# Optimization experiments

Measured on AMD Instinct MI355X. Metric: run time of the kernel, lower is better.

Reference implementation:

```python
import jax, jax.numpy as jnp
import numpy as np

R = 4  # search_radius


def conv3(x, w, b):
    # 3x3 conv, padding=1 (SAME), NCHW / OIHW
    y = jax.lax.conv_general_dilated(x, w, window_strides=(1, 1), padding='SAME',
                                     dimension_numbers=('NCHW', 'OIHW', 'NCHW'))
    return y + b[None, :, None, None]


def bilinear_border(img, x, y):
    # torch F.grid_sample(mode='bilinear', padding_mode='border', align_corners=True)
    # img: (B,C,H,W); x,y: (B,H,W) unnormalized pixel coords
    B, C, H, W = img.shape
    x = jnp.clip(x, 0.0, W - 1.0)
    y = jnp.clip(y, 0.0, H - 1.0)
    x0 = jnp.floor(x)
    y0 = jnp.floor(y)
    x0i = x0.astype(jnp.int32)
    y0i = y0.astype(jnp.int32)
    x1i = jnp.minimum(x0i + 1, W - 1)
    y1i = jnp.minimum(y0i + 1, H - 1)
    wx = (x - x0)[..., None]
    wy = (y - y0)[..., None]
    imgt = jnp.transpose(img, (0, 2, 3, 1))  # (B,H,W,C)
    b = jnp.arange(B)[:, None, None]
    v00 = imgt[b, y0i, x0i]
    v01 = imgt[b, y0i, x1i]
    v10 = imgt[b, y1i, x0i]
    v11 = imgt[b, y1i, x1i]
    out = (v00 * (1 - wx) + v01 * wx) * (1 - wy) + (v10 * (1 - wx) + v11 * wx) * wy
    return jnp.transpose(out, (0, 3, 1, 2))


def _forward(feat1, feat2, initial_flow,
             fW1, fb1, fW2, fb2, fW3, fb3,
             rW1, rb1, rW2, rb2, rW3, rb3, rW4, rb4):
    relu = jax.nn.relu

    def extract(x):
        x = relu(conv3(x, fW1, fb1))
        x = relu(conv3(x, fW2, fb2))
        return relu(conv3(x, fW3, fb3))  # (B, 32, H, W)

    f1 = extract(feat1)
    f2 = extract(feat2)
    B, C, H, W = f1.shape
    yy, xx = jnp.meshgrid(jnp.arange(H, dtype=jnp.float32),
                          jnp.arange(W, dtype=jnp.float32), indexing='ij')
    # warp feat2 by initial flow; align_corners=True normalization cancels -> pixel coords + flow
    f2w = bilinear_border(f2, xx[None] + initial_flow[:, 0], yy[None] + initial_flow[:, 1])
    # search offsets, same order as search_grid.view(2,-1).t(): (dx, dy) row-major over (dy rows)
    coords = jnp.arange(-R, R + 1, dtype=jnp.float32)
    gy, gx = jnp.meshgrid(coords, coords, indexing='ij')
    offs = jnp.stack([gx.reshape(-1), gy.reshape(-1)], axis=1)  # (81, 2)
    xb = jnp.broadcast_to(xx[None], (B, H, W))
    yb = jnp.broadcast_to(yy[None], (B, H, W))

    def cost_fn(off):
        shifted = bilinear_border(f2w, xb + off[0], yb + off[1])
        return jnp.sum(f1 * shifted, axis=1)  # (B,H,W)

    cv = jnp.transpose(jax.lax.map(cost_fn, offs), (1, 0, 2, 3))  # (B,81,H,W)
    h = jnp.concatenate([cv, initial_flow], axis=1)  # (B,83,H,W)
    h = relu(conv3(h, rW1, rb1))
    h = relu(conv3(h, rW2, rb2))
    h = relu(conv3(h, rW3, rb3))
    return initial_flow + conv3(h, rW4, rb4)


def setup_inputs():
    key = jax.random.key(0)
    ks = jax.random.split(key, 12)
    B, H, W = 2, 256, 448
    FC = 64
    CV = (2 * R + 1) ** 2  # 81
    s = 0.05
    d = {}
    d['feat1'] = jax.random.normal(ks[0], (B, 3, H, W), jnp.float32)
    d['feat2'] = jax.random.normal(ks[1], (B, 3, H, W), jnp.float32)
    d['initial_flow'] = jax.random.normal(ks[2], (B, 2, H, W), jnp.float32)
    d['fW1'] = jax.random.normal(ks[3], (FC, 3, 3, 3), jnp.float32) * s
    d['fb1'] = jnp.zeros((FC,), jnp.float32)
    d['fW2'] = jax.random.normal(ks[4], (FC, FC, 3, 3), jnp.float32) * s
    d['fb2'] = jnp.zeros((FC,), jnp.float32)
    d['fW3'] = jax.random.normal(ks[5], (FC // 2, FC, 3, 3), jnp.float32) * s
    d['fb3'] = jnp.zeros((FC // 2,), jnp.float32)
    d['rW1'] = jax.random.normal(ks[6], (128, CV + 2, 3, 3), jnp.float32) * s
    d['rb1'] = jnp.zeros((128,), jnp.float32)
    d['rW2'] = jax.random.normal(ks[7], (128, 128, 3, 3), jnp.float32) * s
    d['rb2'] = jnp.zeros((128,), jnp.float32)
    d['rW3'] = jax.random.normal(ks[8], (64, 128, 3, 3), jnp.float32) * s
    d['rb3'] = jnp.zeros((64,), jnp.float32)
    d['rW4'] = jax.random.normal(ks[9], (2, 64, 3, 3), jnp.float32) * s
    d['rb4'] = jnp.zeros((2,), jnp.float32)
    return d


def reference(feat1, feat2, initial_flow,
              fW1, fb1, fW2, fb2, fW3, fb3,
              rW1, rb1, rW2, rb2, rW3, rb3, rW4, rb4):
    return _forward(feat1, feat2, initial_flow,
                    fW1, fb1, fW2, fb2, fW3, fb3,
                    rW1, rb1, rW2, rb2, rW3, rb3, rW4, rb4)
```

## Files before the change

### kernel.cpp

```cpp
#include <hip/hip_runtime.h>

#define HH 256
#define WW 448
#define HW (HH * WW)

typedef short bf16x8 __attribute__((ext_vector_type(8)));
typedef float f32x4 __attribute__((ext_vector_type(4)));
typedef unsigned int uint32;
typedef unsigned short ushort;

__device__ __forceinline__ ushort f2bf(float f) {
    uint32 u = __float_as_uint(f);
    u += 0x7fffu + ((u >> 16) & 1u);
    return (ushort)(u >> 16);
}

__device__ __forceinline__ void pack_one(
    int i, const float* __restrict__ w, ushort* __restrict__ wp,
    int CinReal, int CinPad, int Cout)
{
    int total = 9 * CinPad * Cout;
    if (i >= total) return;
    int ci = i & 31;
    int rest = i >> 5;
    int n = rest % Cout;
    int rest2 = rest / Cout;
    int KC = CinPad / 32;
    int kc = rest2 % KC;
    int tap = rest2 / KC;
    int cin = kc * 32 + ci;
    float v = (cin < CinReal) ? w[((size_t)n * CinReal + cin) * 9 + tap] : 0.f;
    wp[i] = f2bf(v);
}

__global__ __launch_bounds__(256) void pack_all_k(
    const float* fW2, const float* fW3, const float* rW1,
    const float* rW2, const float* rW3,
    ushort* wp2, ushort* wp3, ushort* wpr1, ushort* wpr2, ushort* wpr3)
{
    int i = blockIdx.x * 256 + threadIdx.x;
    pack_one(i, fW2, wp2, 64, 64, 64);
    pack_one(i, fW3, wp3, 64, 64, 32);
    pack_one(i, rW1, wpr1, 83, 96, 128);
    pack_one(i, rW2, wpr2, 128, 128, 128);
    pack_one(i, rW3, wpr3, 128, 128, 64);
}

template <int CIN, int COUT, int RELU>
__global__ __launch_bounds__(256, 4) void convmfma_k(
    const ushort* __restrict__ in, const ushort* __restrict__ wp,
    const float* __restrict__ bias, ushort* __restrict__ out,
    long inStride, long outStride)
{
    constexpr int KC = CIN / 32;
    constexpr int NPH = (CIN + 63) / 64;
    constexpr int CS = 72;
    constexpr int NG = (COUT >= 128) ? 4 : 2;
    constexpr int WN = (COUT / 16) / NG;
    constexpr int MG = 4 / NG;
    constexpr int WM = 8 / MG;

    __shared__ __align__(16) ushort lds[180 * CS];

    const int tid = threadIdx.x;
    const int x0 = blockIdx.x * 16;
    const int y0 = blockIdx.y * 8;
    in += (size_t)blockIdx.z * inStride;
    out += (size_t)blockIdx.z * outStride;

    const int wv = tid >> 6;
    const int lane = tid & 63;
    const int m = lane & 15;
    const int quad = lane >> 4;
    const int mbase = (wv % MG) * WM;
    const int nbase = (wv / MG) * WN * 16;

    const ushort* ldsA = lds + (mbase * 18 + m) * CS + quad * 8;
    const ushort* wpB = wp + ((size_t)nbase + m) * 32 + quad * 8;

    f32x4 acc[WM][WN];
#pragma unroll
    for (int t = 0; t < WM; ++t)
#pragma unroll
        for (int u = 0; u < WN; ++u)
            acc[t][u] = (f32x4){0.f, 0.f, 0.f, 0.f};

#pragma unroll 1
    for (int ph = 0; ph < NPH; ++ph) {
        const int C = (CIN - ph * 64 >= 64) ? 64 : (CIN - ph * 64);
        const int sh = (C == 64) ? 3 : 2;
        const int ch8 = C >> 3;

        if (ph) __syncthreads();
        for (int i = tid; i < 180 * ch8; i += 256) {
            int p = i >> sh, c8 = i & (ch8 - 1);
            int ry = p / 18, rx = p - ry * 18;
            int gy = y0 + ry - 1, gx = x0 + rx - 1;
            float4 v = make_float4(0.f, 0.f, 0.f, 0.f);
            if (gy >= 0 && gy < HH && gx >= 0 && gx < WW)
                v = *(const float4*)(in + ((size_t)gy * WW + gx) * CIN + ph * 64 + c8 * 8);
            *(float4*)(lds + p * CS + c8 * 8) = v;
        }
        __syncthreads();

        const int KCc = C / 32;
        const ushort* wpP = wpB + (size_t)(ph * 2) * COUT * 32;
#pragma unroll 1
        for (int tap = 0; tap < 9; ++tap) {
            const int ky = tap / 3;
            const int kx = tap - 3 * ky;
            const ushort* wpT = wpP + (size_t)tap * KC * COUT * 32;
#pragma unroll
            for (int kc = 0; kc < 2; ++kc) {
                if (kc >= KCc) break;
                bf16x8 b[WN];
#pragma unroll
                for (int u = 0; u < WN; ++u)
                    b[u] = *(const bf16x8*)(wpT + ((size_t)kc * COUT + u * 16) * 32);
#pragma unroll
                for (int th = 0; th < WM / 4; ++th) {
                    bf16x8 a[4];
#pragma unroll
                    for (int t4 = 0; t4 < 4; ++t4)
                        a[t4] = *(const bf16x8*)(ldsA +
                                ((th * 4 + t4 + ky) * 18 + kx) * CS + kc * 32);
#pragma unroll
                    for (int t4 = 0; t4 < 4; ++t4)
#pragma unroll
                        for (int u = 0; u < WN; ++u)
                            acc[th * 4 + t4][u] =
                                __builtin_amdgcn_mfma_f32_16x16x32_bf16(
                                    a[t4], b[u], acc[th * 4 + t4][u], 0, 0, 0);
                }
            }
        }
    }

#pragma unroll
    for (int u = 0; u < WN; ++u) {
        const int n = nbase + u * 16 + m;
        const float bs = bias[n];
#pragma unroll
        for (int t = 0; t < WM; ++t) {
            const int y = y0 + mbase + t;
#pragma unroll
            for (int r = 0; r < 4; ++r) {
                const int x = x0 + quad * 4 + r;
                float v = acc[t][u][r] + bs;
                if (RELU) v = fmaxf(v, 0.f);
                out[((size_t)y * WW + x) * COUT + n] = f2bf(v);
            }
        }
    }
}

__global__ __launch_bounds__(256) void fconv1_k(
    const float* __restrict__ f1src, const float* __restrict__ f2src,
    const float* __restrict__ w, const float* __restrict__ bias,
    ushort* __restrict__ out, long inStride, long outStride)
{
    __shared__ float wl[1728];
    __shared__ float patch[3][4][18];
    const int tid = threadIdx.x;
    const int x0 = blockIdx.x * 16, y0 = blockIdx.y * 2;
    const int z = blockIdx.z;
    const float* in = ((z & 1) ? f2src : f1src) + (size_t)(z >> 1) * inStride;
    out += (size_t)z * outStride;
    for (int i = tid; i < 1728; i += 256) wl[i] = w[i];
    for (int i = tid; i < 216; i += 256) {
        int ci = i / 72;
        int r = (i - ci * 72) / 18;
        int c = i - ci * 72 - r * 18;
        int gy = y0 + r - 1, gx = x0 + c - 1;
        patch[ci][r][c] = (gy >= 0 && gy < HH && gx >= 0 && gx < WW)
                              ? in[(size_t)ci * HW + gy * WW + gx] : 0.f;
    }
    __syncthreads();
    const int g = tid & 7;
    const int p = tid >> 3;
    const int py = p >> 4, px = p & 15;
    float acc[8];
#pragma unroll
    for (int j = 0; j < 8; ++j) acc[j] = bias[g * 8 + j];
#pragma unroll
    for (int ci = 0; ci < 3; ++ci)
#pragma unroll
        for (int k = 0; k < 9; ++k) {
            const int ky = k / 3, kx = k - 3 * ky;
            const float v = patch[ci][py + ky][px + kx];
#pragma unroll
            for (int j = 0; j < 8; ++j)
                acc[j] = fmaf(v, wl[(g * 8 + j) * 27 + ci * 9 + k], acc[j]);
        }
    ushort ov[8];
#pragma unroll
    for (int j = 0; j < 8; ++j) ov[j] = f2bf(fmaxf(acc[j], 0.f));
    const int y = y0 + py, x = x0 + px;
    *(float4*)(out + ((size_t)y * WW + x) * 64 + g * 8) = *(const float4*)ov;
}

__global__ __launch_bounds__(256) void warp_k(
    const ushort* __restrict__ f2, const float* __restrict__ flow,
    ushort* __restrict__ outp, long fStride, long flowStride, long oStride)
{
    int idx = blockIdx.x * 256 + threadIdx.x;
    if (idx >= HW) return;
    f2 += (size_t)blockIdx.y * fStride;
    flow += (size_t)blockIdx.y * flowStride;
    outp += (size_t)blockIdx.y * oStride;
    int y = idx / WW, x = idx - y * WW;
    float px_ = (float)x + flow[idx];
    float py_ = (float)y + flow[idx + HW];
    px_ = fminf(fmaxf(px_, 0.f), (float)(WW - 1));
    py_ = fminf(fmaxf(py_, 0.f), (float)(HH - 1));
    float fx0 = floorf(px_), fy0 = floorf(py_);
    int xi0 = (int)fx0, yi0 = (int)fy0;
    int xi1 = min(xi0 + 1, WW - 1), yi1 = min(yi0 + 1, HH - 1);
    float wx = px_ - fx0, wy = py_ - fy0;
    float w00 = (1.f - wx) * (1.f - wy), w01 = wx * (1.f - wy);
    float w10 = (1.f - wx) * wy, w11 = wx * wy;

    const uint32* a = (const uint32*)(f2 + ((size_t)yi0 * WW + xi0) * 32);
    const uint32* b = (const uint32*)(f2 + ((size_t)yi0 * WW + xi1) * 32);
    const uint32* c = (const uint32*)(f2 + ((size_t)yi1 * WW + xi0) * 32);
    const uint32* d = (const uint32*)(f2 + ((size_t)yi1 * WW + xi1) * 32);
    uint32 ov[16];
#pragma unroll
    for (int i = 0; i < 16; ++i) {
        uint32 wa = a[i], wb = b[i], wc = c[i], wd = d[i];
        float lo = __uint_as_float(wa << 16) * w00 + __uint_as_float(wb << 16) * w01 +
                   __uint_as_float(wc << 16) * w10 + __uint_as_float(wd << 16) * w11;
        float hi = __uint_as_float(wa & 0xffff0000u) * w00 + __uint_as_float(wb & 0xffff0000u) * w01 +
                   __uint_as_float(wc & 0xffff0000u) * w10 + __uint_as_float(wd & 0xffff0000u) * w11;
        ov[i] = ((uint32)f2bf(hi) << 16) | f2bf(lo);
    }
    uint32* o = (uint32*)(outp + (size_t)idx * 32);
#pragma unroll
    for (int i = 0; i < 16; ++i) o[i] = ov[i];
}

__global__ __launch_bounds__(256) void cost_mfma_k(
    const ushort* __restrict__ f1, const ushort* __restrict__ f2w,
    const float* __restrict__ flow, ushort* __restrict__ hb,
    long f1S, long f2wS, long hbS, long flowS)
{
    const int tid = threadIdx.x;
    const int wv = tid >> 6;
    const int lane = tid & 63;
    const int c = lane & 15;
    const int quad = lane >> 4;
    const int x0 = blockIdx.x * 16;
    const int y = blockIdx.y * 4 + wv;
    f1 += (size_t)blockIdx.z * f1S;
    f2w += (size_t)blockIdx.z * f2wS;
    hb += (size_t)blockIdx.z * hbS;
    flow += (size_t)blockIdx.z * flowS;

    const bf16x8 a = *(const bf16x8*)(f1 + ((size_t)y * WW + x0 + c) * 32 + quad * 8);

    const int xc0 = min(max(x0 - 4 + c, 0), WW - 1);
    const int xc1 = min(max(x0 + 12 + c, 0), WW - 1);

    ushort* hrow = hb + ((size_t)y * WW + x0) * 96;

#pragma unroll 1
    for (int dyi = 0; dyi < 9; ++dyi) {
        const int ys = min(max(y + dyi - 4, 0), HH - 1);
        const bf16x8 b0 = *(const bf16x8*)(f2w + ((size_t)ys * WW + xc0) * 32 + quad * 8);
        const bf16x8 b1 = *(const bf16x8*)(f2w + ((size_t)ys * WW + xc1) * 32 + quad * 8);
        f32x4 s0 = __builtin_amdgcn_mfma_f32_16x16x32_bf16(
            a, b0, (f32x4){0.f, 0.f, 0.f, 0.f}, 0, 0, 0);
        f32x4 s1 = __builtin_amdgcn_mfma_f32_16x16x32_bf16(
            a, b1, (f32x4){0.f, 0.f, 0.f, 0.f}, 0, 0, 0);

        ushort* hq = hrow + dyi * 9;
#pragma unroll
        for (int r = 0; r < 4; ++r) {
            const int m = quad * 4 + r;
            const int d0 = c - m;
            const int d1 = c + 16 - m;
            if (d0 >= 0 && d0 <= 8) hq[(size_t)m * 96 + d0] = f2bf(s0[r]);
            if (d1 <= 8) hq[(size_t)m * 96 + d1] = f2bf(s1[r]);
        }
    }

    if (lane < 16) {
        const int px = y * WW + x0 + lane;
        ushort* hq = hb + (size_t)px * 96;
        hq[81] = f2bf(flow[px]);
        hq[82] = f2bf(flow[px + HW]);
#pragma unroll
        for (int ch = 83; ch < 96; ++ch) hq[ch] = 0;
    }
}

__global__ __launch_bounds__(256) void rconv4_k(
    const ushort* __restrict__ in, const float* __restrict__ w,
    const float* __restrict__ bias, const float* __restrict__ flow,
    float* __restrict__ out, long inStride, long ioStride)
{
    __shared__ float wl[1152];
    for (int i = threadIdx.x; i < 1152; i += 256) wl[i] = w[i];
    __syncthreads();
    in += (size_t)blockIdx.y * inStride;
    flow += (size_t)blockIdx.y * ioStride;
    out += (size_t)blockIdx.y * ioStride;
    int px = blockIdx.x * 256 + threadIdx.x;
    if (px >= HW) return;
    int y = px / WW, x = px - y * WW;
    float a0 = bias[0], a1 = bias[1];
    for (int ky = 0; ky < 3; ++ky) {
        int gy = y + ky - 1;
        if (gy < 0 || gy >= HH) continue;
        for (int kx = 0; kx < 3; ++kx) {
            int gx = x + kx - 1;
            if (gx < 0 || gx >= WW) continue;
            const uint32* p = (const uint32*)(in + ((size_t)gy * WW + gx) * 64);
            int tap = ky * 3 + kx;
#pragma unroll
            for (int i = 0; i < 32; ++i) {
                uint32 wv = p[i];
                float lo = __uint_as_float(wv << 16);
                float hi = __uint_as_float(wv & 0xffff0000u);
                a0 = fmaf(lo, wl[(2 * i) * 9 + tap], a0);
                a0 = fmaf(hi, wl[(2 * i + 1) * 9 + tap], a0);
                a1 = fmaf(lo, wl[576 + (2 * i) * 9 + tap], a1);
                a1 = fmaf(hi, wl[576 + (2 * i + 1) * 9 + tap], a1);
            }
        }
    }
    out[px] = flow[px] + a0;
    out[px + HW] = flow[px + HW] + a1;
}

extern "C" void kernel_launch(void* const* d_in, const int* in_sizes, int n_in,
                              void* d_out, int out_size, void* d_ws, size_t ws_size,
                              hipStream_t stream)
{
    (void)in_sizes; (void)n_in; (void)out_size;
    const float* feat1 = (const float*)d_in[0];
    const float* feat2 = (const float*)d_in[1];
    const float* iflow = (const float*)d_in[2];
    const float* fW1 = (const float*)d_in[3];  const float* fb1 = (const float*)d_in[4];
    const float* fW2 = (const float*)d_in[5];  const float* fb2 = (const float*)d_in[6];
    const float* fW3 = (const float*)d_in[7];  const float* fb3 = (const float*)d_in[8];
    const float* rW1 = (const float*)d_in[9];  const float* rb1 = (const float*)d_in[10];
    const float* rW2 = (const float*)d_in[11]; const float* rb2 = (const float*)d_in[12];
    const float* rW3 = (const float*)d_in[13]; const float* rb3 = (const float*)d_in[14];
    const float* rW4 = (const float*)d_in[15]; const float* rb4 = (const float*)d_in[16];
    float* out = (float*)d_out;

    const size_t P = (size_t)HW;
    const size_t WTOT = (size_t)9 * (64 * 64 + 64 * 32 + 96 * 128 + 128 * 128 + 128 * 64);
    ushort* ws0 = (ushort*)d_ws;
    ushort* wp2  = ws0;
    ushort* wp3  = wp2 + 9 * 64 * 64;
    ushort* wpr1 = wp3 + 9 * 64 * 32;
    ushort* wpr2 = wpr1 + 9 * 96 * 128;
    ushort* wpr3 = wpr2 + 9 * 128 * 128;
    ushort* arena = ws0 + WTOT;

    const bool merged = ws_size >= (WTOT + 640 * P) * sizeof(ushort);
    const int nb = merged ? 2 : 1;
    const int nloop = merged ? 1 : 2;

    ushort* XA = arena;
    ushort* XB = XA + (size_t)(nb * 128) * P;
    ushort* F  = XB + (size_t)(nb * 128) * P;
    ushort* F2W = XA;
    ushort* Hb  = XA + (size_t)(nb * 32) * P;
    ushort* R1  = XB;
    ushort* R2  = XA;
    ushort* R3  = F;

    const dim3 blk(256);
    pack_all_k<<<dim3((9 * 128 * 128 + 255) / 256), blk, 0, stream>>>(
        fW2, fW3, rW1, rW2, rW3, wp2, wp3, wpr1, wpr2, wpr3);

    const dim3 gConvX(WW / 16, HH / 8, nb * 2);
    const dim3 gConvB(WW / 16, HH / 8, nb);
    const dim3 gF1(WW / 16, HH / 2, nb * 2);
    const dim3 gCost(WW / 16, HH / 4, nb);
    const int gPix = (HW + 255) / 256;

    for (int lb = 0; lb < nloop; ++lb) {
        const float* f1in = feat1 + (size_t)lb * 3 * P;
        const float* f2in = feat2 + (size_t)lb * 3 * P;
        const float* flw  = iflow + (size_t)lb * 2 * P;
        float* outb = out + (size_t)lb * 2 * P;

        fconv1_k<<<gF1, blk, 0, stream>>>(f1in, f2in, fW1, fb1, XA, 3 * (long)P, 64 * (long)P);
        convmfma_k<64, 64, 1><<<gConvX, blk, 0, stream>>>(XA, wp2, fb2, XB, 64 * (long)P, 64 * (long)P);
        convmfma_k<64, 32, 1><<<gConvX, blk, 0, stream>>>(XB, wp3, fb3, F, 64 * (long)P, 32 * (long)P);

        warp_k<<<dim3(gPix, nb), blk, 0, stream>>>(F + 32 * P, flw, F2W,
                                                   64 * (long)P, 2 * (long)P, 32 * (long)P);

        cost_mfma_k<<<gCost, blk, 0, stream>>>(F, F2W, flw, Hb,
                                               64 * (long)P, 32 * (long)P, 96 * (long)P, 2 * (long)P);

        convmfma_k<96, 128, 1><<<gConvB, blk, 0, stream>>>(Hb, wpr1, rb1, R1, 96 * (long)P, 128 * (long)P);
        convmfma_k<128, 128, 1><<<gConvB, blk, 0, stream>>>(R1, wpr2, rb2, R2, 128 * (long)P, 128 * (long)P);
        convmfma_k<128, 64, 1><<<gConvB, blk, 0, stream>>>(R2, wpr3, rb3, R3, 128 * (long)P, 64 * (long)P);
        rconv4_k<<<dim3(gPix, nb), blk, 0, stream>>>(R3, rW4, rb4, flw, outb, 64 * (long)P, 2 * (long)P);
    }
}
```

Baseline: 488.0 us.

## Double conv tile width to 32x8 pixels and remap waves across halves

The implicit-GEMM conv kernel now covers a 32x8 output tile instead of 16x8, staging a 34x10 halo in LDS, and waves are redistributed so each computes more M-tiles with fewer N-groups. The aim is to lower halo overhead and reuse each loaded weight fragment across more pixel tiles, improving the ratio of MFMA work to global and LDS traffic. In exchange, LDS use nearly doubles and the accumulator register count grows, so the occupancy hint in launch bounds drops to 2-3 blocks. The grid width is halved to match.

```diff
diff --git a/kernel.cpp b/kernel.cpp
--- a/kernel.cpp
+++ b/kernel.cpp
@@ -47,7 +47,7 @@
 }
 
 template <int CIN, int COUT, int RELU>
-__global__ __launch_bounds__(256, 4) void convmfma_k(
+__global__ __launch_bounds__(256, (COUT >= 128 ? 2 : 3)) void convmfma_k(
     const ushort* __restrict__ in, const ushort* __restrict__ wp,
     const float* __restrict__ bias, ushort* __restrict__ out,
     long inStride, long outStride)
@@ -55,15 +55,15 @@
     constexpr int KC = CIN / 32;
     constexpr int NPH = (CIN + 63) / 64;
     constexpr int CS = 72;
-    constexpr int NG = (COUT >= 128) ? 4 : 2;
-    constexpr int WN = (COUT / 16) / NG;
-    constexpr int MG = 4 / NG;
-    constexpr int WM = 8 / MG;
-
-    __shared__ __align__(16) ushort lds[180 * CS];
+    constexpr int NGW = (COUT >= 64) ? 2 : 1;
+    constexpr int MGW = 4 / NGW;
+    constexpr int WMT = 16 / MGW;
+    constexpr int WN = (COUT / 16) / NGW;
+
+    __shared__ __align__(16) ushort lds[340 * CS];
 
     const int tid = threadIdx.x;
-    const int x0 = blockIdx.x * 16;
+    const int x0 = blockIdx.x * 32;
     const int y0 = blockIdx.y * 8;
     in += (size_t)blockIdx.z * inStride;
     out += (size_t)blockIdx.z * outStride;
@@ -72,15 +72,15 @@
     const int lane = tid & 63;
     const int m = lane & 15;
     const int quad = lane >> 4;
-    const int mbase = (wv % MG) * WM;
-    const int nbase = (wv / MG) * WN * 16;
-
-    const ushort* ldsA = lds + (mbase * 18 + m) * CS + quad * 8;
+    const int mbase = (wv % MGW) * WMT;
+    const int nbase = (wv / MGW) * WN * 16;
+
+    const ushort* ldsA = lds + (size_t)m * CS + quad * 8;
     const ushort* wpB = wp + ((size_t)nbase + m) * 32 + quad * 8;
 
-    f32x4 acc[WM][WN];
-#pragma unroll
-    for (int t = 0; t < WM; ++t)
+    f32x4 acc[WMT][WN];
+#pragma unroll
+    for (int t = 0; t < WMT; ++t)
 #pragma unroll
         for (int u = 0; u < WN; ++u)
             acc[t][u] = (f32x4){0.f, 0.f, 0.f, 0.f};
@@ -92,14 +92,14 @@
         const int ch8 = C >> 3;
 
         if (ph) __syncthreads();
-        for (int i = tid; i < 180 * ch8; i += 256) {
+        for (int i = tid; i < 340 * ch8; i += 256) {
             int p = i >> sh, c8 = i & (ch8 - 1);
-            int ry = p / 18, rx = p - ry * 18;
+            int ry = p / 34, rx = p - ry * 34;
             int gy = y0 + ry - 1, gx = x0 + rx - 1;
             float4 v = make_float4(0.f, 0.f, 0.f, 0.f);
             if (gy >= 0 && gy < HH && gx >= 0 && gx < WW)
                 v = *(const float4*)(in + ((size_t)gy * WW + gx) * CIN + ph * 64 + c8 * 8);
-            *(float4*)(lds + p * CS + c8 * 8) = v;
+            *(float4*)(lds + (size_t)p * CS + c8 * 8) = v;
         }
         __syncthreads();
 
@@ -118,19 +118,21 @@
                 for (int u = 0; u < WN; ++u)
                     b[u] = *(const bf16x8*)(wpT + ((size_t)kc * COUT + u * 16) * 32);
 #pragma unroll
-                for (int th = 0; th < WM / 4; ++th) {
+                for (int ch = 0; ch < WMT; ch += 4) {
                     bf16x8 a[4];
 #pragma unroll
-                    for (int t4 = 0; t4 < 4; ++t4)
-                        a[t4] = *(const bf16x8*)(ldsA +
-                                ((th * 4 + t4 + ky) * 18 + kx) * CS + kc * 32);
-#pragma unroll
-                    for (int t4 = 0; t4 < 4; ++t4)
+                    for (int j = 0; j < 4; ++j) {
+                        const int mt = mbase + ch + j;
+                        const int row = mt >> 1, half = mt & 1;
+                        a[j] = *(const bf16x8*)(ldsA +
+                                ((row + ky) * 34 + half * 16 + kx) * CS + kc * 32);
+                    }
+#pragma unroll
+                    for (int j = 0; j < 4; ++j)
 #pragma unroll
                         for (int u = 0; u < WN; ++u)
-                            acc[th * 4 + t4][u] =
-                                __builtin_amdgcn_mfma_f32_16x16x32_bf16(
-                                    a[t4], b[u], acc[th * 4 + t4][u], 0, 0, 0);
+                            acc[ch + j][u] = __builtin_amdgcn_mfma_f32_16x16x32_bf16(
+                                a[j], b[u], acc[ch + j][u], 0, 0, 0);
                 }
             }
         }
@@ -141,11 +143,13 @@
         const int n = nbase + u * 16 + m;
         const float bs = bias[n];
 #pragma unroll
-        for (int t = 0; t < WM; ++t) {
-            const int y = y0 + mbase + t;
+        for (int t = 0; t < WMT; ++t) {
+            const int mt = mbase + t;
+            const int y = y0 + (mt >> 1);
+            const int xh = x0 + (mt & 1) * 16;
 #pragma unroll
             for (int r = 0; r < 4; ++r) {
-                const int x = x0 + quad * 4 + r;
+                const int x = xh + quad * 4 + r;
                 float v = acc[t][u][r] + bs;
                 if (RELU) v = fmaxf(v, 0.f);
                 out[((size_t)y * WW + x) * COUT + n] = f2bf(v);
@@ -377,8 +381,8 @@
     pack_all_k<<<dim3((9 * 128 * 128 + 255) / 256), blk, 0, stream>>>(
         fW2, fW3, rW1, rW2, rW3, wp2, wp3, wpr1, wpr2, wpr3);
 
-    const dim3 gConvX(WW / 16, HH / 8, nb * 2);
-    const dim3 gConvB(WW / 16, HH / 8, nb);
+    const dim3 gConvX(WW / 32, HH / 8, nb * 2);
+    const dim3 gConvB(WW / 32, HH / 8, nb);
     const dim3 gF1(WW / 16, HH / 2, nb * 2);
     const dim3 gCost(WW / 16, HH / 4, nb);
     const int gPix = (HW + 255) / 256;
```

Result: slower. 502.7 us (+3.0%).
